# Kernel tuning notes

Hardware: AMD Instinct MI355X
Metric: run time of the kernel (lower is better)

## Reference

```python
import jax, jax.numpy as jnp
import numpy as np

C0 = 32   # number of 0e (scalar) channels
C1 = 16   # number of 1o (vector) channels
NG = 1024 # num_graphs
N = 300000
F = C0 * (C0 + 1) // 2 + C1 * (C1 + 1) // 2  # 664 invariant outputs of TensorSquare->0e


def setup_inputs() -> dict:
    key = jax.random.key(0)
    k1, k2, k3 = jax.random.split(key, 3)
    node_ft = jax.random.normal(k1, (N, C0 + 3 * C1), dtype=jnp.float32)
    batch_index = jnp.sort(jax.random.randint(k2, (N,), 0, NG, dtype=jnp.int32))
    # o3.Linear-style init: normal / sqrt(fan_in)
    W = jax.random.normal(k3, (F, 1), dtype=jnp.float32) / np.float32(np.sqrt(F))
    return {"node_ft": node_ft, "batch_index": batch_index, "num_graphs": NG, "W": W}


def tensor_square_0e(node_ft):
    # Equivariant tensor square keeping only 0e (invariant) outputs:
    #  - symmetric products of scalar channels s_i * s_j (i<=j)
    #  - dot products of vector channels v_i . v_j (i<=j), component-normalized
    s = node_ft[:, :C0]                      # [N, C0]
    v = node_ft[:, C0:].reshape(-1, C1, 3)   # [N, C1, 3]
    i0, j0 = jnp.triu_indices(C0)
    i1, j1 = jnp.triu_indices(C1)
    ts_s = s[:, i0] * s[:, j0]                                  # [N, 528]
    vdot = jnp.einsum('nic,njc->nij', v, v) / jnp.float32(np.sqrt(3.0))
    ts_v = vdot[:, i1, j1]                                      # [N, 136]
    return jnp.concatenate([ts_s, ts_v], axis=1)                # [N, 664]


def reference(node_ft, batch_index, num_graphs, W):
    x = tensor_square_0e(node_ft)            # [N, F]
    x = jax.nn.selu(x)
    x = x @ W                                # [N, 1] attention logits (1x0e)
    ex = jnp.exp(x)                          # [N, 1]
    z = jax.ops.segment_sum(ex, batch_index, num_segments=num_graphs)  # [G, 1]
    attn = ex / z[batch_index]               # segment softmax weights [N, 1]
    out = jax.ops.segment_sum(node_ft * attn, batch_index, num_segments=num_graphs)
    return out                               # [G, C0 + 3*C1]
```

## Files before the change

kernel.cpp:

```cpp
#include <hip/hip_runtime.h>


typedef float f2 __attribute__((ext_vector_type(2)));

#define C0 32
#define C1 16
#define NODE_F 80
#define NG_CONST 1024

#define SELU_SCALE 1.0507009873554804934193349852946
#define SELU_ALPHA 1.6732632423543772848170429916717
#define LOG2E      1.4426950408889634073599246810019

#define CS_SCALE 1.2011224087864498f
#define CV_SCALE 0.91271231102878545f

__global__ __launch_bounds__(256) void pass1_logits(
    const float* __restrict__ nf, const float* __restrict__ W,
    float* __restrict__ ex_out, int N)
{
    const int t  = threadIdx.x;
    const int na = blockIdx.x * 512 + 2 * t;
    if (na >= N) return;
    const int  nb  = na + 1;
    const bool nbv = (nb < N);
    const int  nbe = nbv ? nb : na;

    const float* rowa = nf + (size_t)na * NODE_F;
    const float* rowb = nf + (size_t)nbe * NODE_F;

    f2 acc1[2], acc2[2];
    acc1[0] = 0.f; acc1[1] = 0.f; acc2[0] = 0.f; acc2[1] = 0.f;
    int k = 0;

    {
        f2 ss2[C0];
        const float4* pa = (const float4*)rowa;
        const float4* pb = (const float4*)rowb;
        #pragma unroll
        for (int q = 0; q < C0 / 4; ++q) {
            float4 va = pa[q], vb = pb[q];
            ss2[4*q+0] = f2{va.x, vb.x} * CS_SCALE;
            ss2[4*q+1] = f2{va.y, vb.y} * CS_SCALE;
            ss2[4*q+2] = f2{va.z, vb.z} * CS_SCALE;
            ss2[4*q+3] = f2{va.w, vb.w} * CS_SCALE;
        }
        #pragma unroll
        for (int i = 0; i < C0; ++i) {
            #pragma unroll
            for (int j = i; j < C0; ++j) {
                f2 f = ss2[i] * ss2[j];
                f2 p = __builtin_elementwise_max(f, (f2)0.f);
                f2 m = __builtin_elementwise_min(f, (f2)0.f);
                f2 e; e.x = __builtin_amdgcn_exp2f(m.x);
                      e.y = __builtin_amdgcn_exp2f(m.y);
                f2 w = W[k];
                acc1[k & 1] = __builtin_elementwise_fma(w, p, acc1[k & 1]);
                acc2[k & 1] = __builtin_elementwise_fma(w, e, acc2[k & 1]);
                ++k;
            }
        }
    }

    {
        f2 vs2[3 * C1];
        const float4* pa = (const float4*)(rowa + C0);
        const float4* pb = (const float4*)(rowb + C0);
        #pragma unroll
        for (int q = 0; q < (3 * C1) / 4; ++q) {
            float4 va = pa[q], vb = pb[q];
            vs2[4*q+0] = f2{va.x, vb.x} * CV_SCALE;
            vs2[4*q+1] = f2{va.y, vb.y} * CV_SCALE;
            vs2[4*q+2] = f2{va.z, vb.z} * CV_SCALE;
            vs2[4*q+3] = f2{va.w, vb.w} * CV_SCALE;
        }
        #pragma unroll
        for (int i = 0; i < C1; ++i) {
            #pragma unroll
            for (int j = i; j < C1; ++j) {
                f2 f = vs2[3*i] * vs2[3*j];
                f = __builtin_elementwise_fma(vs2[3*i+1], vs2[3*j+1], f);
                f = __builtin_elementwise_fma(vs2[3*i+2], vs2[3*j+2], f);
                f2 p = __builtin_elementwise_max(f, (f2)0.f);
                f2 m = __builtin_elementwise_min(f, (f2)0.f);
                f2 e; e.x = __builtin_amdgcn_exp2f(m.x);
                      e.y = __builtin_amdgcn_exp2f(m.y);
                f2 w = W[k];
                acc1[k & 1] = __builtin_elementwise_fma(w, p, acc1[k & 1]);
                acc2[k & 1] = __builtin_elementwise_fma(w, e, acc2[k & 1]);
                ++k;
            }
        }
    }

    f2 a1 = acc1[0] + acc1[1];
    f2 a2 = acc2[0] + acc2[1];
    f2 l2 = a1 * (float)SELU_SCALE;
    l2 = __builtin_elementwise_fma((f2)(float)(SELU_SCALE * SELU_ALPHA * LOG2E), a2, l2);
    f2 exv; exv.x = __builtin_amdgcn_exp2f(l2.x);
            exv.y = __builtin_amdgcn_exp2f(l2.y);

    if (nbv) *(f2*)(ex_out + na) = exv;
    else     ex_out[na] = exv.x;
}

__global__ __launch_bounds__(256) void seg_bounds_kernel(
    const int* __restrict__ bi, int* __restrict__ bounds, int N)
{
    const int g = blockIdx.x * blockDim.x + threadIdx.x;
    if (g > NG_CONST) return;
    int lo = 0, hi = N;
    while (lo < hi) {
        int mid = (lo + hi) >> 1;
        if (bi[mid] < g) lo = mid + 1; else hi = mid;
    }
    bounds[g] = lo;
}

#define P2T 320

__global__ __launch_bounds__(P2T) void pass2_pool(
    const float* __restrict__ nf, const float* __restrict__ ex,
    const int* __restrict__ bounds, float* __restrict__ out)
{
    __shared__ float  zred[P2T];
    __shared__ float4 red4[P2T];
    const int g = blockIdx.x;
    const int tid = threadIdx.x;
    const int start = bounds[g];
    const int end   = bounds[g + 1];

    float part = 0.0f;
    for (int n = start + tid; n < end; n += P2T) part += ex[n];
    zred[tid] = part;
    __syncthreads();
    if (tid < 64) zred[tid] += zred[tid + 256];
    __syncthreads();
    #pragma unroll
    for (int s = 128; s > 0; s >>= 1) {
        if (tid < s) zred[tid] += zred[tid + s];
        __syncthreads();
    }
    const float z = zred[0];
    const float inv_z = (z > 0.0f) ? (1.0f / z) : 0.0f;

    const int no = tid / 20;
    const int c4 = tid % 20;
    const float4* nf4 = (const float4*)nf;
    float4 acc = make_float4(0.f, 0.f, 0.f, 0.f);
    for (int n = start + no; n < end; n += 16) {
        float  w = ex[n];
        float4 v = nf4[(size_t)n * 20 + c4];
        acc.x = fmaf(v.x, w, acc.x);
        acc.y = fmaf(v.y, w, acc.y);
        acc.z = fmaf(v.z, w, acc.z);
        acc.w = fmaf(v.w, w, acc.w);
    }
    red4[tid] = acc;
    __syncthreads();
    #pragma unroll
    for (int s = 8; s > 0; s >>= 1) {
        if (no < s) {
            float4 o = red4[tid + s * 20];
            red4[tid].x += o.x; red4[tid].y += o.y;
            red4[tid].z += o.z; red4[tid].w += o.w;
        }
        __syncthreads();
    }
    if (tid < 20) {
        float4 r = red4[tid];
        r.x *= inv_z; r.y *= inv_z; r.z *= inv_z; r.w *= inv_z;
        ((float4*)(out + (size_t)g * NODE_F))[tid] = r;
    }
}

extern "C" void kernel_launch(void* const* d_in, const int* in_sizes, int n_in,
                              void* d_out, int out_size, void* d_ws, size_t ws_size,
                              hipStream_t stream) {
    const float* nf = (const float*)d_in[0];
    const int*   bi = (const int*)d_in[1];
    const float* W  = (const float*)d_in[3];
    float* out = (float*)d_out;

    const int N = in_sizes[0] / NODE_F;
    float* ex     = (float*)d_ws;
    int*   bounds = (int*)d_ws + N;

    hipLaunchKernelGGL(seg_bounds_kernel, dim3((NG_CONST + 256) / 256), dim3(256),
                       0, stream, bi, bounds, N);
    hipLaunchKernelGGL(pass1_logits, dim3((N + 511) / 512), dim3(256),
                       0, stream, nf, W, ex, N);
    hipLaunchKernelGGL(pass2_pool, dim3(NG_CONST), dim3(P2T),
                       0, stream, nf, ex, bounds, out);
}
```

Before: 196.1 us.

## Stage rows through LDS, pack channel pairs per thread, fuse softmax denominator into pooling

```diff
diff --git a/kernel.cpp b/kernel.cpp
--- a/kernel.cpp
+++ b/kernel.cpp
@@ -15,93 +15,116 @@
 #define CS_SCALE 1.2011224087864498f
 #define CV_SCALE 0.91271231102878545f
 
-__global__ __launch_bounds__(256) void pass1_logits(
+#define KS(i, j) ((i) * C0 - ((i) * ((i) -1)) / 2 + ((j) - (i)))
+#define KV(i, j) (528 + (i) * C1 - ((i) * ((i) -1)) / 2 + ((j) - (i)))
+
+__global__ __launch_bounds__(256, 4) void pass1_logits(
     const float* __restrict__ nf, const float* __restrict__ W,
     float* __restrict__ ex_out, int N)
 {
-    const int t  = threadIdx.x;
-    const int na = blockIdx.x * 512 + 2 * t;
-    if (na >= N) return;
-    const int  nb  = na + 1;
-    const bool nbv = (nb < N);
-    const int  nbe = nbv ? nb : na;
-
-    const float* rowa = nf + (size_t)na * NODE_F;
-    const float* rowb = nf + (size_t)nbe * NODE_F;
-
-    f2 acc1[2], acc2[2];
-    acc1[0] = 0.f; acc1[1] = 0.f; acc2[0] = 0.f; acc2[1] = 0.f;
-    int k = 0;
+    __shared__ float4 buf[128 * 20];
+    const int tid = threadIdx.x;
+    const int base_row = blockIdx.x * 256;
+    const int total4 = N * 20;
+    const float4* g4 = (const float4*)nf;
+
+    float4 row4[20];
+    const int half = tid >> 7;
+    const int r    = tid & 127;
+
+    #pragma unroll
+    for (int it = 0; it < 10; ++it) {
+        int g = base_row * 20 + it * 256 + tid;
+        buf[it * 256 + tid] = g4[g < total4 ? g : 0];
+    }
+    __syncthreads();
+    if (half == 0) {
+        const float4* src = &buf[r * 20];
+        #pragma unroll
+        for (int q = 0; q < 20; ++q) row4[q] = src[q];
+    }
+    __syncthreads();
+    #pragma unroll
+    for (int it = 0; it < 10; ++it) {
+        int g = (base_row + 128) * 20 + it * 256 + tid;
+        buf[it * 256 + tid] = g4[g < total4 ? g : 0];
+    }
+    __syncthreads();
+    if (half == 1) {
+        const float4* src = &buf[r * 20];
+        #pragma unroll
+        for (int q = 0; q < 20; ++q) row4[q] = src[q];
+    }
+
+    const float* row = (const float*)row4;
+
+    f2 accA[2], accB[2];
+    accA[0] = 0.f; accA[1] = 0.f; accB[0] = 0.f; accB[1] = 0.f;
 
     {
-        f2 ss2[C0];
-        const float4* pa = (const float4*)rowa;
-        const float4* pb = (const float4*)rowb;
-        #pragma unroll
-        for (int q = 0; q < C0 / 4; ++q) {
-            float4 va = pa[q], vb = pb[q];
-            ss2[4*q+0] = f2{va.x, vb.x} * CS_SCALE;
-            ss2[4*q+1] = f2{va.y, vb.y} * CS_SCALE;
-            ss2[4*q+2] = f2{va.z, vb.z} * CS_SCALE;
-            ss2[4*q+3] = f2{va.w, vb.w} * CS_SCALE;
-        }
+        f2 s2[C0 / 2];
+        #pragma unroll
+        for (int q = 0; q < C0 / 2; ++q)
+            s2[q] = f2{row[2 * q], row[2 * q + 1]} * CS_SCALE;
+
         #pragma unroll
         for (int i = 0; i < C0; ++i) {
+            const float si = (i & 1) ? s2[i >> 1].y : s2[i >> 1].x;
+            const f2 si2 = f2{si, si};
             #pragma unroll
-            for (int j = i; j < C0; ++j) {
-                f2 f = ss2[i] * ss2[j];
+            for (int q = i / 2; q < C0 / 2; ++q) {
+                f2 f = si2 * s2[q];
                 f2 p = __builtin_elementwise_max(f, (f2)0.f);
                 f2 m = __builtin_elementwise_min(f, (f2)0.f);
                 f2 e; e.x = __builtin_amdgcn_exp2f(m.x);
                       e.y = __builtin_amdgcn_exp2f(m.y);
-                f2 w = W[k];
-                acc1[k & 1] = __builtin_elementwise_fma(w, p, acc1[k & 1]);
-                acc2[k & 1] = __builtin_elementwise_fma(w, e, acc2[k & 1]);
-                ++k;
+                f2 w;
+                w.x = (2 * q >= i) ? W[KS(i, 2 * q)] : 0.0f;
+                w.y = W[KS(i, 2 * q + 1)];
+                accA[q & 1] = __builtin_elementwise_fma(w, p, accA[q & 1]);
+                accB[q & 1] = __builtin_elementwise_fma(w, e, accB[q & 1]);
             }
         }
     }
 
     {
-        f2 vs2[3 * C1];
-        const float4* pa = (const float4*)(rowa + C0);
-        const float4* pb = (const float4*)(rowb + C0);
-        #pragma unroll
-        for (int q = 0; q < (3 * C1) / 4; ++q) {
-            float4 va = pa[q], vb = pb[q];
-            vs2[4*q+0] = f2{va.x, vb.x} * CV_SCALE;
-            vs2[4*q+1] = f2{va.y, vb.y} * CV_SCALE;
-            vs2[4*q+2] = f2{va.z, vb.z} * CV_SCALE;
-            vs2[4*q+3] = f2{va.w, vb.w} * CV_SCALE;
+        f2 vp[C1 / 2][3];
+        #pragma unroll
+        for (int q = 0; q < C1 / 2; ++q) {
+            #pragma unroll
+            for (int c = 0; c < 3; ++c)
+                vp[q][c] = f2{row[C0 + 6 * q + c], row[C0 + 6 * q + 3 + c]} * CV_SCALE;
         }
         #pragma unroll
         for (int i = 0; i < C1; ++i) {
+            const int iq = i >> 1;
+            float vi0 = (i & 1) ? vp[iq][0].y : vp[iq][0].x;
+            float vi1 = (i & 1) ? vp[iq][1].y : vp[iq][1].x;
+            float vi2 = (i & 1) ? vp[iq][2].y : vp[iq][2].x;
             #pragma unroll
-            for (int j = i; j < C1; ++j) {
-                f2 f = vs2[3*i] * vs2[3*j];
-                f = __builtin_elementwise_fma(vs2[3*i+1], vs2[3*j+1], f);
-                f = __builtin_elementwise_fma(vs2[3*i+2], vs2[3*j+2], f);
+            for (int q = i / 2; q < C1 / 2; ++q) {
+                f2 f = f2{vi0, vi0} * vp[q][0];
+                f = __builtin_elementwise_fma(f2{vi1, vi1}, vp[q][1], f);
+                f = __builtin_elementwise_fma(f2{vi2, vi2}, vp[q][2], f);
                 f2 p = __builtin_elementwise_max(f, (f2)0.f);
                 f2 m = __builtin_elementwise_min(f, (f2)0.f);
                 f2 e; e.x = __builtin_amdgcn_exp2f(m.x);
                       e.y = __builtin_amdgcn_exp2f(m.y);
-                f2 w = W[k];
-                acc1[k & 1] = __builtin_elementwise_fma(w, p, acc1[k & 1]);
-                acc2[k & 1] = __builtin_elementwise_fma(w, e, acc2[k & 1]);
-                ++k;
+                f2 w;
+                w.x = (2 * q >= i) ? W[KV(i, 2 * q)] : 0.0f;
+                w.y = W[KV(i, 2 * q + 1)];
+                accA[q & 1] = __builtin_elementwise_fma(w, p, accA[q & 1]);
+                accB[q & 1] = __builtin_elementwise_fma(w, e, accB[q & 1]);
             }
         }
     }
 
-    f2 a1 = acc1[0] + acc1[1];
-    f2 a2 = acc2[0] + acc2[1];
-    f2 l2 = a1 * (float)SELU_SCALE;
-    l2 = __builtin_elementwise_fma((f2)(float)(SELU_SCALE * SELU_ALPHA * LOG2E), a2, l2);
-    f2 exv; exv.x = __builtin_amdgcn_exp2f(l2.x);
-            exv.y = __builtin_amdgcn_exp2f(l2.y);
-
-    if (nbv) *(f2*)(ex_out + na) = exv;
-    else     ex_out[na] = exv.x;
+    const float A1 = accA[0].x + accA[0].y + accA[1].x + accA[1].y;
+    const float A2 = accB[0].x + accB[0].y + accB[1].x + accB[1].y;
+    const float l2 = fmaf((float)SELU_SCALE, A1,
+                          (float)(SELU_SCALE * SELU_ALPHA * LOG2E) * A2);
+    const int n = base_row + tid;
+    if (n < N) ex_out[n] = __builtin_amdgcn_exp2f(l2);
 }
 
 __global__ __launch_bounds__(256) void seg_bounds_kernel(
@@ -117,57 +140,64 @@
     bounds[g] = lo;
 }
 
-#define P2T 320
+#define P2T 640
 
 __global__ __launch_bounds__(P2T) void pass2_pool(
     const float* __restrict__ nf, const float* __restrict__ ex,
     const int* __restrict__ bounds, float* __restrict__ out)
 {
+    __shared__ float4 red4[P2T];
     __shared__ float  zred[P2T];
-    __shared__ float4 red4[P2T];
     const int g = blockIdx.x;
     const int tid = threadIdx.x;
     const int start = bounds[g];
     const int end   = bounds[g + 1];
 
-    float part = 0.0f;
-    for (int n = start + tid; n < end; n += P2T) part += ex[n];
-    zred[tid] = part;
-    __syncthreads();
-    if (tid < 64) zred[tid] += zred[tid + 256];
-    __syncthreads();
-    #pragma unroll
-    for (int s = 128; s > 0; s >>= 1) {
-        if (tid < s) zred[tid] += zred[tid + s];
-        __syncthreads();
-    }
-    const float z = zred[0];
-    const float inv_z = (z > 0.0f) ? (1.0f / z) : 0.0f;
-
     const int no = tid / 20;
     const int c4 = tid % 20;
     const float4* nf4 = (const float4*)nf;
-    float4 acc = make_float4(0.f, 0.f, 0.f, 0.f);
-    for (int n = start + no; n < end; n += 16) {
-        float  w = ex[n];
-        float4 v = nf4[(size_t)n * 20 + c4];
-        acc.x = fmaf(v.x, w, acc.x);
-        acc.y = fmaf(v.y, w, acc.y);
-        acc.z = fmaf(v.z, w, acc.z);
-        acc.w = fmaf(v.w, w, acc.w);
-    }
-    red4[tid] = acc;
+
+    float4 a0 = make_float4(0.f, 0.f, 0.f, 0.f), a1 = a0;
+    float  z0 = 0.f, z1 = 0.f;
+    int n = start + no;
+    for (; n + 32 < end; n += 64) {
+        float  w0 = ex[n];
+        float4 v0 = nf4[(size_t)n * 20 + c4];
+        float  w1 = ex[n + 32];
+        float4 v1 = nf4[(size_t)(n + 32) * 20 + c4];
+        a0.x = fmaf(v0.x, w0, a0.x); a0.y = fmaf(v0.y, w0, a0.y);
+        a0.z = fmaf(v0.z, w0, a0.z); a0.w = fmaf(v0.w, w0, a0.w);
+        z0 += w0;
+        a1.x = fmaf(v1.x, w1, a1.x); a1.y = fmaf(v1.y, w1, a1.y);
+        a1.z = fmaf(v1.z, w1, a1.z); a1.w = fmaf(v1.w, w1, a1.w);
+        z1 += w1;
+    }
+    if (n < end) {
+        float  w0 = ex[n];
+        float4 v0 = nf4[(size_t)n * 20 + c4];
+        a0.x = fmaf(v0.x, w0, a0.x); a0.y = fmaf(v0.y, w0, a0.y);
+        a0.z = fmaf(v0.z, w0, a0.z); a0.w = fmaf(v0.w, w0, a0.w);
+        z0 += w0;
+    }
+    a0.x += a1.x; a0.y += a1.y; a0.z += a1.z; a0.w += a1.w;
+    z0 += z1;
+
+    red4[tid] = a0;
+    zred[tid] = z0;
     __syncthreads();
     #pragma unroll
-    for (int s = 8; s > 0; s >>= 1) {
+    for (int s = 16; s > 0; s >>= 1) {
         if (no < s) {
             float4 o = red4[tid + s * 20];
             red4[tid].x += o.x; red4[tid].y += o.y;
             red4[tid].z += o.z; red4[tid].w += o.w;
+            zred[tid] += zred[tid + s * 20];
         }
         __syncthreads();
     }
     if (tid < 20) {
+        float z = zred[tid];
+        float inv_z = (z > 0.0f) ? (1.0f / z) : 0.0f;
         float4 r = red4[tid];
         r.x *= inv_z; r.y *= inv_z; r.z *= inv_z; r.w *= inv_z;
         ((float4*)(out + (size_t)g * NODE_F))[tid] = r;
@@ -188,7 +218,7 @@
 
     hipLaunchKernelGGL(seg_bounds_kernel, dim3((NG_CONST + 256) / 256), dim3(256),
                        0, stream, bi, bounds, N);
-    hipLaunchKernelGGL(pass1_logits, dim3((N + 511) / 512), dim3(256),
+    hipLaunchKernelGGL(pass1_logits, dim3((N + 255) / 256), dim3(256),
                        0, stream, nf, W, ex, N);
     hipLaunchKernelGGL(pass2_pool, dim3(NG_CONST), dim3(P2T),
                        0, stream, nf, ex, bounds, out);
```

Measured after the change: 201.9 us. +3.0%, slower.
